# Kernel optimization log

Hardware: AMD Instinct MI355X
Metric: run time of the kernel (lower is better)

Reference implementation:

```python
import jax, jax.numpy as jnp
import numpy as np


def setup_inputs() -> dict:
    key = jax.random.key(0)
    ks = jax.random.split(key, 10)
    B, S, I, H = 32, 512, 256, 512
    stdv = 1.0 / np.sqrt(H)
    u = lambda k, shape: jax.random.uniform(k, shape, jnp.float32, -stdv, stdv)
    return {
        "inputs": jax.random.normal(ks[0], (B, S, I), jnp.float32),
        "h0": jax.random.normal(ks[1], (2, B, H), jnp.float32),
        "weight_ih_f": u(ks[2], (H, I)),
        "weight_hh_f": u(ks[3], (H, H)),
        "bias_ih_f": u(ks[4], (H,)),
        "bias_hh_f": u(ks[5], (H,)),
        "weight_ih_b": u(ks[6], (H, I)),
        "weight_hh_b": u(ks[7], (H, H)),
        "bias_ih_b": u(ks[8], (H,)),
        "bias_hh_b": u(ks[9], (H,)),
    }


def _rnn_direction(x_proj, h0, weight_hh):
    # x_proj: [S, B, H] precomputed input projection + biases; h0: [B, H]
    def step(h, xp):
        h_new = jax.nn.relu(xp + h @ weight_hh.T)
        return h_new, h_new
    hn, outs = jax.lax.scan(step, h0, x_proj)
    return hn, outs  # outs: [S, B, H]


def reference(inputs, h0, weight_ih_f, weight_hh_f, bias_ih_f, bias_hh_f,
              weight_ih_b, weight_hh_b, bias_ih_b, bias_hh_b):
    # inputs: [B, S, I]; h0: [2, B, H]
    x_sbI = jnp.swapaxes(inputs, 0, 1)  # [S, B, I]
    # Hoist the input GEMM out of the recurrence (math identical).
    xp_f = x_sbI @ weight_ih_f.T + bias_ih_f + bias_hh_f  # [S, B, H]
    xp_b = x_sbI @ weight_ih_b.T + bias_ih_b + bias_hh_b
    hn_f, outs_f = _rnn_direction(xp_f, h0[0], weight_hh_f)
    # backward direction: scan reversed sequence, then flip outputs back
    hn_b, outs_b_rev = _rnn_direction(xp_b[::-1], h0[1], weight_hh_b)
    outs_b = outs_b_rev[::-1]
    outputs = jnp.concatenate((outs_f, outs_b), axis=-1)  # [S, B, 2H]
    outputs = jnp.swapaxes(outputs, 0, 1)  # [B, S, 2H]
    hn = jnp.stack((hn_f, hn_b), axis=0)  # [2, B, H]
    return outputs, hn
```

## Files before the change

kernel.cpp:

```cpp
#include <hip/hip_runtime.h>
#include <stdint.h>

#define B_ 32
#define S_ 512
#define I_ 256
#define H_ 512
#define OUTW 1024
#define OUTS_ELEMS (B_*S_*OUTW)

typedef _Float16 f16;
typedef _Float16 half2_t __attribute__((ext_vector_type(2)));

__device__ __forceinline__ float fdot2(uint32_t a, uint32_t b, float c){
#if __has_builtin(__builtin_amdgcn_fdot2)
  return __builtin_amdgcn_fdot2(__builtin_bit_cast(half2_t, a),
                                __builtin_bit_cast(half2_t, b), c, false);
#else
  half2_t ha = __builtin_bit_cast(half2_t, a);
  half2_t hb = __builtin_bit_cast(half2_t, b);
  return c + (float)ha.x*(float)hb.x + (float)ha.y*(float)hb.y;
#endif
}

__device__ __forceinline__ uint32_t packf16(float x, float y){
  union { f16 h[2]; uint32_t u; } z;
  z.h[0] = (f16)x; z.h[1] = (f16)y;
  return z.u;
}

template<int CTRL>
__device__ __forceinline__ float dpp_xor_add(float x){
  int v = __builtin_amdgcn_update_dpp(0, __float_as_int(x), CTRL, 0xF, 0xF, true);
  return x + __int_as_float(v);
}

__global__ __launch_bounds__(256) void cvt_w_kernel(const float* __restrict__ wf,
                                                    const float* __restrict__ wb,
                                                    f16* __restrict__ out){
  int i = blockIdx.x*256 + threadIdx.x;
  const float* src = (i < 32768) ? wf : wb;
  int base = (i & 32767) * 8;
  float4 a = *(const float4*)(src + base);
  float4 c = *(const float4*)(src + base + 4);
  uint4 o;
  o.x = packf16(a.x, a.y); o.y = packf16(a.z, a.w);
  o.z = packf16(c.x, c.y); o.w = packf16(c.z, c.w);
  *(uint4*)(out + (size_t)i*8) = o;
}

#define PTM 128
#define PTN 64
#define PTK 32
__global__ __launch_bounds__(256) void proj_kernel(
    const float* __restrict__ x,
    const float* __restrict__ wihf, const float* __restrict__ wihb,
    const float* __restrict__ bihf, const float* __restrict__ bhhf,
    const float* __restrict__ bihb, const float* __restrict__ bhhb,
    float* __restrict__ out)
{
  __shared__ float As[PTK][132];
  __shared__ float Bs[PTK][68];
  const int tid = threadIdx.x;
  const int row0 = blockIdx.x * PTM;
  const int j0   = blockIdx.y * PTN;
  const int dir  = (j0 >= 512) ? 1 : 0;
  const int jl0  = j0 - dir*512;
  const float* wih = dir ? wihb : wihf;
  const float* bi  = dir ? bihb : bihf;
  const float* bh  = dir ? bhhb : bhhf;

  const int ty = tid >> 4, tx = tid & 15;
  float acc[8][4];
#pragma unroll
  for (int i=0;i<8;i++)
#pragma unroll
    for (int j=0;j<4;j++) acc[i][j] = 0.f;

  float bias[4];
#pragma unroll
  for (int jj=0;jj<4;jj++){ int jl = jl0 + tx*4 + jj; bias[jj] = bi[jl] + bh[jl]; }

  for (int k0 = 0; k0 < I_; k0 += PTK){
    {
      int r = tid >> 1, kh = (tid & 1) * 16;
      int rg = row0 + r; int bb = rg & 31, tt = rg >> 5;
      const float* ap = x + ((size_t)bb*S_ + tt)*I_ + k0 + kh;
#pragma unroll
      for (int u=0;u<4;u++){
        float4 v = *(const float4*)(ap + u*4);
        As[kh+u*4+0][r] = v.x; As[kh+u*4+1][r] = v.y;
        As[kh+u*4+2][r] = v.z; As[kh+u*4+3][r] = v.w;
      }
    }
    {
      int jr = tid >> 2, kh = (tid & 3) * 8;
      const float* bp = wih + (size_t)(jl0 + jr)*I_ + k0 + kh;
#pragma unroll
      for (int u=0;u<2;u++){
        float4 v = *(const float4*)(bp + u*4);
        Bs[kh+u*4+0][jr] = v.x; Bs[kh+u*4+1][jr] = v.y;
        Bs[kh+u*4+2][jr] = v.z; Bs[kh+u*4+3][jr] = v.w;
      }
    }
    __syncthreads();
#pragma unroll 8
    for (int kk=0; kk<PTK; ++kk){
      const float4 a0 = *(const float4*)&As[kk][ty*8+0];
      const float4 a1 = *(const float4*)&As[kk][ty*8+4];
      const float4 bq = *(const float4*)&Bs[kk][tx*4];
      const float av[8] = {a0.x,a0.y,a0.z,a0.w,a1.x,a1.y,a1.z,a1.w};
      const float bv[4] = {bq.x,bq.y,bq.z,bq.w};
#pragma unroll
      for (int i=0;i<8;i++)
#pragma unroll
        for (int j=0;j<4;j++) acc[i][j] = fmaf(av[i], bv[j], acc[i][j]);
    }
    __syncthreads();
  }
#pragma unroll
  for (int i=0;i<8;i++){
    int rg = row0 + ty*8 + i; int bb = rg & 31, tt = rg >> 5;
    float* op = out + ((size_t)bb*S_ + tt)*OUTW + j0 + tx*4;
    float4 v = {acc[i][0]+bias[0], acc[i][1]+bias[1], acc[i][2]+bias[2], acc[i][3]+bias[3]};
    *(float4*)op = v;
  }
}

#define LDSW 131072
#define LDS_TOTAL (LDSW + 2048)

#define ROWR(ACC, R) \
  ACC = fdot2(wreg[R][c*4+0], hv.x, ACC); \
  ACC = fdot2(wreg[R][c*4+1], hv.y, ACC); \
  ACC = fdot2(wreg[R][c*4+2], hv.z, ACC); \
  ACC = fdot2(wreg[R][c*4+3], hv.w, ACC);

#define ROWL(ACC, WV) \
  ACC = fdot2(WV.x, hv.x, ACC); ACC = fdot2(WV.y, hv.y, ACC); \
  ACC = fdot2(WV.z, hv.z, ACC); ACC = fdot2(WV.w, hv.w, ACC);

__global__ __launch_bounds__(512, 2) void rnn_kernel(
    const f16* __restrict__ Wall,
    const float* __restrict__ h0,
    float* dout)
{
  extern __shared__ char lds[];
  const int tid = threadIdx.x;
  const int dir = blockIdx.x >> 5;
  const int b   = blockIdx.x & 31;
  const int jg  = tid >> 3;
  const int ks  = tid & 7;
  const f16* W = Wall + (size_t)dir * (H_*(size_t)H_);
  float* outs = dout + (size_t)b * (S_*OUTW) + dir * H_;
  float* hn   = dout + (size_t)OUTS_ELEMS + ((size_t)dir*B_ + b) * H_;

  uint32_t wreg[6][32];
#pragma unroll
  for (int m=0;m<6;m++){
    const uint4* src = (const uint4*)(W + ((size_t)(jg + 64*m))*H_ + ks*64);
#pragma unroll
    for (int c=0;c<8;c++){
      uint4 v = src[c];
      wreg[m][c*4+0]=v.x; wreg[m][c*4+1]=v.y;
      wreg[m][c*4+2]=v.z; wreg[m][c*4+3]=v.w;
    }
  }
  {
    int r = tid >> 2, q = tid & 3;
    const uint4* src = (const uint4*)(W + ((size_t)(384 + r))*H_);
#pragma unroll
    for (int cc=0;cc<16;cc++){
      int c = q*16 + cc;
      int kss = c >> 3;
      int ii2 = (c & 7) ^ ((kss ^ r) & 7);
      *((uint4*)(lds + r*1024 + kss*128 + ii2*16)) = src[c];
    }
  }
  {
    int j = tid;
    int off = (j>>6)*128 + ((((j>>3)&7) ^ (j>>6)) & 7)*16 + (j&7)*2;
    *((f16*)(lds + LDSW + off)) = (f16)h0[((size_t)dir*B_ + b)*H_ + j];
  }
  __syncthreads();

  const int jfin = jg + 64*ks;
  const int sw16 = ((ks ^ jg) & 7) << 4;
  const int w6o = jg*1024 + ks*128 + sw16;
  const int w7o = (64+jg)*1024 + ks*128 + sw16;
  const int hxo = ks*128 + (ks<<4);
  const int hwoff = (jfin>>6)*128 + ((((jfin>>3)&7) ^ (jfin>>6)) & 7)*16 + (jfin&7)*2;

  float h_last = 0.f;
  int cur = 0;
  for (int s=0; s<S_; ++s){
    const int t = dir ? (S_-1-s) : s;
    float* xo = outs + (size_t)t*OUTW;
    float xpv = xo[jfin];
    float acc0=0.f,acc1=0.f,acc2=0.f,acc3=0.f,acc4=0.f,acc5=0.f,acc6=0.f,acc7=0.f;
    const char* hbase = lds + LDSW + (cur<<10);
#pragma unroll
    for (int c=0;c<8;c++){
      const uint4 hv = *(const uint4*)(hbase + (hxo ^ (c<<4)));
      const uint4 w6 = *(const uint4*)(lds + (w6o ^ (c<<4)));
      const uint4 w7 = *(const uint4*)(lds + (w7o ^ (c<<4)));
      ROWR(acc0, 0) ROWR(acc1, 1) ROWR(acc2, 2)
      ROWR(acc3, 3) ROWR(acc4, 4) ROWR(acc5, 5)
      ROWL(acc6, w6) ROWL(acc7, w7)
    }
    acc0 = dpp_xor_add<0xB1>(acc0); acc1 = dpp_xor_add<0xB1>(acc1);
    acc2 = dpp_xor_add<0xB1>(acc2); acc3 = dpp_xor_add<0xB1>(acc3);
    acc4 = dpp_xor_add<0xB1>(acc4); acc5 = dpp_xor_add<0xB1>(acc5);
    acc6 = dpp_xor_add<0xB1>(acc6); acc7 = dpp_xor_add<0xB1>(acc7);
    acc0 = dpp_xor_add<0x4E>(acc0); acc1 = dpp_xor_add<0x4E>(acc1);
    acc2 = dpp_xor_add<0x4E>(acc2); acc3 = dpp_xor_add<0x4E>(acc3);
    acc4 = dpp_xor_add<0x4E>(acc4); acc5 = dpp_xor_add<0x4E>(acc5);
    acc6 = dpp_xor_add<0x4E>(acc6); acc7 = dpp_xor_add<0x4E>(acc7);
    const int k3 = ks & 3;
    float slo = (k3==0)?acc0:(k3==1)?acc1:(k3==2)?acc2:acc3;
    float shi = (k3==0)?acc4:(k3==1)?acc5:(k3==2)?acc6:acc7;
    float own  = (ks<4)? slo : shi;
    float give = (ks<4)? shi : slo;
    float tot = own + __shfl_xor(give, 4);
    float hnew = fmaxf(xpv + tot, 0.f);
    xo[jfin] = hnew;
    h_last = hnew;
    *((f16*)(lds + LDSW + ((cur^1)<<10) + hwoff)) = (f16)hnew;
    asm volatile("s_waitcnt lgkmcnt(0)" ::: "memory");
    __builtin_amdgcn_s_barrier();
    cur ^= 1;
  }
  hn[jfin] = h_last;
}

extern "C" void kernel_launch(void* const* d_in, const int* in_sizes, int n_in,
                              void* d_out, int out_size, void* d_ws, size_t ws_size,
                              hipStream_t stream){
  const float* x    = (const float*)d_in[0];
  const float* h0   = (const float*)d_in[1];
  const float* wihf = (const float*)d_in[2];
  const float* whhf = (const float*)d_in[3];
  const float* bihf = (const float*)d_in[4];
  const float* bhhf = (const float*)d_in[5];
  const float* wihb = (const float*)d_in[6];
  const float* whhb = (const float*)d_in[7];
  const float* bihb = (const float*)d_in[8];
  const float* bhhb = (const float*)d_in[9];
  float* out = (float*)d_out;
  f16* wf16 = (f16*)d_ws;

  cvt_w_kernel<<<256, 256, 0, stream>>>(whhf, whhb, wf16);
  proj_kernel<<<dim3(128, 16), 256, 0, stream>>>(x, wihf, wihb, bihf, bhhf, bihb, bhhb, out);
  (void)hipFuncSetAttribute((const void*)rnn_kernel,
                            hipFuncAttributeMaxDynamicSharedMemorySize, LDS_TOTAL);
  rnn_kernel<<<64, 512, LDS_TOTAL, stream>>>(wf16, h0, out);
}
```

Before: 792.0 us.

## Split each RNN sequence across two workgroups exchanging hidden halves via global mailboxes

Each (direction, batch) recurrence is now handled by two workgroups, each owning half of the hidden units. Each workgroup keeps its weight slice entirely in registers, dropping the large LDS weight buffer, and swaps its new hidden half with its partner every step through tagged global-memory mailboxes polled with atomic loads. The point is to halve per-step dot-product work per workgroup and use twice as many CUs. The cost is cross-CU spin-wait latency on every step, and the scheme relies on both partners being resident at the same time. Mailbox tags are 16-bit and nothing resets them between launches, so stale values from a previous call could match.

```diff
diff --git a/kernel.cpp b/kernel.cpp
--- a/kernel.cpp
+++ b/kernel.cpp
@@ -32,6 +32,10 @@
 __device__ __forceinline__ float dpp_xor_add(float x){
   int v = __builtin_amdgcn_update_dpp(0, __float_as_int(x), CTRL, 0xF, 0xF, true);
   return x + __int_as_float(v);
+}
+
+__device__ __forceinline__ int swz16(int chunk){
+  return (chunk & ~7) | ((chunk ^ (chunk >> 3)) & 7);
 }
 
 __global__ __launch_bounds__(256) void cvt_w_kernel(const float* __restrict__ wf,
@@ -126,110 +130,129 @@
   }
 }
 
-#define LDSW 131072
-#define LDS_TOTAL (LDSW + 2048)
-
-#define ROWR(ACC, R) \
-  ACC = fdot2(wreg[R][c*4+0], hv.x, ACC); \
-  ACC = fdot2(wreg[R][c*4+1], hv.y, ACC); \
-  ACC = fdot2(wreg[R][c*4+2], hv.z, ACC); \
-  ACC = fdot2(wreg[R][c*4+3], hv.w, ACC);
-
-#define ROWL(ACC, WV) \
-  ACC = fdot2(WV.x, hv.x, ACC); ACC = fdot2(WV.y, hv.y, ACC); \
-  ACC = fdot2(WV.z, hv.z, ACC); ACC = fdot2(WV.w, hv.w, ACC);
+#define MAIL_OFF_U32 (1u<<18)
 
 __global__ __launch_bounds__(512, 2) void rnn_kernel(
     const f16* __restrict__ Wall,
     const float* __restrict__ h0,
-    float* dout)
+    float* dout, uint32_t* mailbase)
 {
-  extern __shared__ char lds[];
-  const int tid = threadIdx.x;
-  const int dir = blockIdx.x >> 5;
-  const int b   = blockIdx.x & 31;
-  const int jg  = tid >> 3;
-  const int ks  = tid & 7;
-  const f16* W = Wall + (size_t)dir * (H_*(size_t)H_);
-  float* outs = dout + (size_t)b * (S_*OUTW) + dir * H_;
-  float* hn   = dout + (size_t)OUTS_ELEMS + ((size_t)dir*B_ + b) * H_;
-
-  uint32_t wreg[6][32];
-#pragma unroll
-  for (int m=0;m<6;m++){
-    const uint4* src = (const uint4*)(W + ((size_t)(jg + 64*m))*H_ + ks*64);
-#pragma unroll
-    for (int c=0;c<8;c++){
-      uint4 v = src[c];
-      wreg[m][c*4+0]=v.x; wreg[m][c*4+1]=v.y;
-      wreg[m][c*4+2]=v.z; wreg[m][c*4+3]=v.w;
-    }
-  }
+  __shared__ char lds[2048];
+  const int tid  = threadIdx.x;
+  const int g    = blockIdx.x;
+  const int dir  = g >> 6;
+  const int b    = (g >> 1) & 31;
+  const int half = g & 1;
+  const int jg   = tid >> 3;
+  const int ks   = tid & 7;
+  const int k3   = ks & 3;
+  const bool owner = (ks < 4);
+  const int jl   = jg + 64*k3;
+
+  const f16* Wd = Wall + (size_t)dir * (H_*(size_t)H_);
+  float* outs = dout + (size_t)b * (S_*OUTW);
+  const int col = dir*512 + half*256 + jl;
+  float* hn = dout + (size_t)OUTS_ELEMS + ((size_t)dir*B_ + b) * H_;
+
+  uint32_t* mail = mailbase;
+  const int pairid = dir*32 + b;
+  uint32_t* mw = mail + ((size_t)pairid*2 + half) * 512;
+  uint32_t* mr = mail + ((size_t)pairid*2 + (half^1)) * 512;
+
+  uint32_t wL[4][16], wR[4][16];
+#pragma unroll
+  for (int r=0;r<4;r++){
+    const f16* row = Wd + (size_t)(half*256 + jg + 64*r) * H_;
+    const uint4* pL = (const uint4*)(row + half*256 + ks*32);
+    const uint4* pR = (const uint4*)(row + (half^1)*256 + ks*32);
+#pragma unroll
+    for (int q=0;q<4;q++){
+      uint4 v = pL[q];
+      wL[r][q*4+0]=v.x; wL[r][q*4+1]=v.y; wL[r][q*4+2]=v.z; wL[r][q*4+3]=v.w;
+      uint4 u = pR[q];
+      wR[r][q*4+0]=u.x; wR[r][q*4+1]=u.y; wR[r][q*4+2]=u.z; wR[r][q*4+3]=u.w;
+    }
+  }
+
+  int oL[4], oR[4];
+#pragma unroll
+  for (int q=0;q<4;q++){
+    oL[q] = swz16(half*32     + ks*4 + q) * 16;
+    oR[q] = swz16((half^1)*32 + ks*4 + q) * 16;
+  }
+  const int kO = half*256 + jl;
+  const int oO = swz16(kO>>3)*16 + (kO&7)*2;
+  const int kS = (half^1)*256 + tid;
+  const int oS = swz16(kS>>3)*16 + (kS&7)*2;
+
   {
-    int r = tid >> 2, q = tid & 3;
-    const uint4* src = (const uint4*)(W + ((size_t)(384 + r))*H_);
-#pragma unroll
-    for (int cc=0;cc<16;cc++){
-      int c = q*16 + cc;
-      int kss = c >> 3;
-      int ii2 = (c & 7) ^ ((kss ^ r) & 7);
-      *((uint4*)(lds + r*1024 + kss*128 + ii2*16)) = src[c];
-    }
-  }
-  {
-    int j = tid;
-    int off = (j>>6)*128 + ((((j>>3)&7) ^ (j>>6)) & 7)*16 + (j&7)*2;
-    *((f16*)(lds + LDSW + off)) = (f16)h0[((size_t)dir*B_ + b)*H_ + j];
+    int k = tid;
+    int off = swz16(k>>3)*16 + (k&7)*2;
+    *(f16*)(lds + 1024 + off) = (f16)h0[((size_t)dir*B_ + b)*H_ + k];
   }
   __syncthreads();
 
-  const int jfin = jg + 64*ks;
-  const int sw16 = ((ks ^ jg) & 7) << 4;
-  const int w6o = jg*1024 + ks*128 + sw16;
-  const int w7o = (64+jg)*1024 + ks*128 + sw16;
-  const int hxo = ks*128 + (ks<<4);
-  const int hwoff = (jfin>>6)*128 + ((((jfin>>3)&7) ^ (jfin>>6)) & 7)*16 + (jfin&7)*2;
-
-  float h_last = 0.f;
-  int cur = 0;
   for (int s=0; s<S_; ++s){
     const int t = dir ? (S_-1-s) : s;
+    const int P = (s+1)&1;
+    char* hb = lds + P*1024;
     float* xo = outs + (size_t)t*OUTW;
-    float xpv = xo[jfin];
-    float acc0=0.f,acc1=0.f,acc2=0.f,acc3=0.f,acc4=0.f,acc5=0.f,acc6=0.f,acc7=0.f;
-    const char* hbase = lds + LDSW + (cur<<10);
-#pragma unroll
-    for (int c=0;c<8;c++){
-      const uint4 hv = *(const uint4*)(hbase + (hxo ^ (c<<4)));
-      const uint4 w6 = *(const uint4*)(lds + (w6o ^ (c<<4)));
-      const uint4 w7 = *(const uint4*)(lds + (w7o ^ (c<<4)));
-      ROWR(acc0, 0) ROWR(acc1, 1) ROWR(acc2, 2)
-      ROWR(acc3, 3) ROWR(acc4, 4) ROWR(acc5, 5)
-      ROWL(acc6, w6) ROWL(acc7, w7)
-    }
-    acc0 = dpp_xor_add<0xB1>(acc0); acc1 = dpp_xor_add<0xB1>(acc1);
-    acc2 = dpp_xor_add<0xB1>(acc2); acc3 = dpp_xor_add<0xB1>(acc3);
-    acc4 = dpp_xor_add<0xB1>(acc4); acc5 = dpp_xor_add<0xB1>(acc5);
-    acc6 = dpp_xor_add<0xB1>(acc6); acc7 = dpp_xor_add<0xB1>(acc7);
-    acc0 = dpp_xor_add<0x4E>(acc0); acc1 = dpp_xor_add<0x4E>(acc1);
-    acc2 = dpp_xor_add<0x4E>(acc2); acc3 = dpp_xor_add<0x4E>(acc3);
-    acc4 = dpp_xor_add<0x4E>(acc4); acc5 = dpp_xor_add<0x4E>(acc5);
-    acc6 = dpp_xor_add<0x4E>(acc6); acc7 = dpp_xor_add<0x4E>(acc7);
-    const int k3 = ks & 3;
-    float slo = (k3==0)?acc0:(k3==1)?acc1:(k3==2)?acc2:acc3;
-    float shi = (k3==0)?acc4:(k3==1)?acc5:(k3==2)?acc6:acc7;
-    float own  = (ks<4)? slo : shi;
-    float give = (ks<4)? shi : slo;
-    float tot = own + __shfl_xor(give, 4);
-    float hnew = fmaxf(xpv + tot, 0.f);
-    xo[jfin] = hnew;
-    h_last = hnew;
-    *((f16*)(lds + LDSW + ((cur^1)<<10) + hwoff)) = (f16)hnew;
-    asm volatile("s_waitcnt lgkmcnt(0)" ::: "memory");
-    __builtin_amdgcn_s_barrier();
-    cur ^= 1;
-  }
-  hn[jfin] = h_last;
+    float xpv = 0.f;
+    if (owner) xpv = xo[col];
+
+    float a0=0.f, a1=0.f, a2=0.f, a3=0.f;
+#pragma unroll
+    for (int q=0;q<4;q++){
+      const uint4 hv = *(const uint4*)(hb + oL[q]);
+      a0 = fdot2(wL[0][q*4+0],hv.x,a0); a0 = fdot2(wL[0][q*4+1],hv.y,a0);
+      a0 = fdot2(wL[0][q*4+2],hv.z,a0); a0 = fdot2(wL[0][q*4+3],hv.w,a0);
+      a1 = fdot2(wL[1][q*4+0],hv.x,a1); a1 = fdot2(wL[1][q*4+1],hv.y,a1);
+      a1 = fdot2(wL[1][q*4+2],hv.z,a1); a1 = fdot2(wL[1][q*4+3],hv.w,a1);
+      a2 = fdot2(wL[2][q*4+0],hv.x,a2); a2 = fdot2(wL[2][q*4+1],hv.y,a2);
+      a2 = fdot2(wL[2][q*4+2],hv.z,a2); a2 = fdot2(wL[2][q*4+3],hv.w,a2);
+      a3 = fdot2(wL[3][q*4+0],hv.x,a3); a3 = fdot2(wL[3][q*4+1],hv.y,a3);
+      a3 = fdot2(wL[3][q*4+2],hv.z,a3); a3 = fdot2(wL[3][q*4+3],hv.w,a3);
+    }
+    if (s > 0 && tid < 256){
+      const uint32_t tag = (uint32_t)s & 0xffffu;
+      uint32_t v;
+      do {
+        v = __hip_atomic_load(&mr[P*256 + tid], __ATOMIC_RELAXED, __HIP_MEMORY_SCOPE_AGENT);
+      } while ((v & 0xffffu) != tag);
+      uint16_t hb16 = (uint16_t)(v >> 16);
+      *(f16*)(hb + oS) = __builtin_bit_cast(f16, hb16);
+    }
+    __syncthreads();
+#pragma unroll
+    for (int q=0;q<4;q++){
+      const uint4 hv = *(const uint4*)(hb + oR[q]);
+      a0 = fdot2(wR[0][q*4+0],hv.x,a0); a0 = fdot2(wR[0][q*4+1],hv.y,a0);
+      a0 = fdot2(wR[0][q*4+2],hv.z,a0); a0 = fdot2(wR[0][q*4+3],hv.w,a0);
+      a1 = fdot2(wR[1][q*4+0],hv.x,a1); a1 = fdot2(wR[1][q*4+1],hv.y,a1);
+      a1 = fdot2(wR[1][q*4+2],hv.z,a1); a1 = fdot2(wR[1][q*4+3],hv.w,a1);
+      a2 = fdot2(wR[2][q*4+0],hv.x,a2); a2 = fdot2(wR[2][q*4+1],hv.y,a2);
+      a2 = fdot2(wR[2][q*4+2],hv.z,a2); a2 = fdot2(wR[2][q*4+3],hv.w,a2);
+      a3 = fdot2(wR[3][q*4+0],hv.x,a3); a3 = fdot2(wR[3][q*4+1],hv.y,a3);
+      a3 = fdot2(wR[3][q*4+2],hv.z,a3); a3 = fdot2(wR[3][q*4+3],hv.w,a3);
+    }
+    a0 = dpp_xor_add<0xB1>(a0); a1 = dpp_xor_add<0xB1>(a1);
+    a2 = dpp_xor_add<0xB1>(a2); a3 = dpp_xor_add<0xB1>(a3);
+    a0 = dpp_xor_add<0x4E>(a0); a1 = dpp_xor_add<0x4E>(a1);
+    a2 = dpp_xor_add<0x4E>(a2); a3 = dpp_xor_add<0x4E>(a3);
+    float own = (k3==0)?a0:(k3==1)?a1:(k3==2)?a2:a3;
+    float tot = own + __shfl_xor(own, 4);
+
+    if (owner){
+      float h = fmaxf(xpv + tot, 0.f);
+      xo[col] = h;
+      if (s == S_-1) hn[half*256 + jl] = h;
+      uint16_t hb16 = __builtin_bit_cast(uint16_t, (f16)h);
+      *(f16*)(lds + (P^1)*1024 + oO) = __builtin_bit_cast(f16, hb16);
+      uint32_t val = ((uint32_t)hb16 << 16) | ((uint32_t)(s+1) & 0xffffu);
+      __hip_atomic_store(&mw[(P^1)*256 + jl], val, __ATOMIC_RELAXED, __HIP_MEMORY_SCOPE_AGENT);
+    }
+    __syncthreads();
+  }
 }
 
 extern "C" void kernel_launch(void* const* d_in, const int* in_sizes, int n_in,
@@ -247,10 +270,9 @@
   const float* bhhb = (const float*)d_in[9];
   float* out = (float*)d_out;
   f16* wf16 = (f16*)d_ws;
+  uint32_t* mail = (uint32_t*)d_ws + MAIL_OFF_U32;
 
   cvt_w_kernel<<<256, 256, 0, stream>>>(whhf, whhb, wf16);
   proj_kernel<<<dim3(128, 16), 256, 0, stream>>>(x, wihf, wihb, bihf, bhhf, bihb, bhhb, out);
-  (void)hipFuncSetAttribute((const void*)rnn_kernel,
-                            hipFuncAttributeMaxDynamicSharedMemorySize, LDS_TOTAL);
-  rnn_kernel<<<64, 512, LDS_TOTAL, stream>>>(wf16, h0, out);
-}
+  rnn_kernel<<<128, 512, 0, stream>>>(wf16, h0, out, mail);
+}
```

After: 660.7 us. 16.6% less time.
